# Performance work log

Hardware: AMD Instinct MI355X
Metric: run time of the kernel (lower is better)

Reference implementation:

```python
import jax, jax.numpy as jnp
import numpy as np

N_NODES = 200000
N_EDGES = 800000
N_GRAPHS = 4000
D_N = 35      # len(ATOM_VOCAB)=17 + 18
IN_CH = 8     # hardcoded in_channels
EMB = 256     # args.emb_size * 2
HID = 128     # args.emb_size (pred head hidden)


def setup_inputs() -> dict:
    key = jax.random.key(0)
    ks = jax.random.split(key, 16)
    s = lambda fan_in: 1.0 / np.sqrt(fan_in)
    x = jax.random.normal(ks[0], (N_NODES, D_N), dtype=jnp.float32)
    src = jax.random.randint(ks[1], (N_EDGES,), 0, N_NODES, dtype=jnp.int32)
    dst = jax.random.randint(ks[2], (N_EDGES,), 0, N_NODES, dtype=jnp.int32)
    seg = jnp.sort(jax.random.randint(ks[3], (N_NODES,), 0, N_GRAPHS, dtype=jnp.int32))
    return {
        "x": x, "src": src, "dst": dst, "seg": seg,
        # emb_linear (no bias): d_n -> 8
        "W_emb": jax.random.uniform(ks[4], (IN_CH, D_N), jnp.float32, -s(D_N), s(D_N)),
        # GCN layer 1: 8 -> 256 (agg='sum', residual=False)
        "W1": jax.random.uniform(ks[5], (EMB, IN_CH), jnp.float32, -s(IN_CH), s(IN_CH)),
        "b1": jnp.zeros((EMB,), jnp.float32),
        # GCN layers 2,3: 256 -> 256 (residual=True)
        "W2": jax.random.uniform(ks[6], (EMB, EMB), jnp.float32, -s(EMB), s(EMB)),
        "b2": jnp.zeros((EMB,), jnp.float32),
        "W3": jax.random.uniform(ks[7], (EMB, EMB), jnp.float32, -s(EMB), s(EMB)),
        "b3": jnp.zeros((EMB,), jnp.float32),
        # pred head: Linear(256,128,bias=False) -> ReLU -> Linear(128,1)
        "Wp1": jax.random.uniform(ks[8], (HID, EMB), jnp.float32, -s(EMB), s(EMB)),
        "Wp2": jax.random.uniform(ks[9], (1, HID), jnp.float32, -s(HID), s(HID)),
        "bp2": jnp.zeros((1,), jnp.float32),
    }


def _gcn_layer(h, src, dst, W, b, residual):
    # gather source node feats along edges, scatter-sum into destinations
    m = jax.ops.segment_sum(h[src], dst, num_segments=N_NODES)  # [N, d]
    out = jax.nn.relu(m @ W.T + b)
    return out + h if residual else out


def reference(x, src, dst, seg, W_emb, W1, b1, W2, b2, W3, b3, Wp1, Wp2, bp2):
    h = x @ W_emb.T                                   # [N, 8]
    h = _gcn_layer(h, src, dst, W1, b1, residual=False)  # [N, 256]
    h = _gcn_layer(h, src, dst, W2, b2, residual=True)
    h = _gcn_layer(h, src, dst, W3, b3, residual=True)
    g = jax.ops.segment_sum(h, seg, num_segments=N_GRAPHS)  # sum pooling [B, 256]
    pred = jax.nn.relu(g @ Wp1.T) @ Wp2.T + bp2       # [B, 1]
    return pred
```

## Files before the change

### kernel.cpp

```cpp
#include <hip/hip_runtime.h>
#include <hip/hip_bf16.h>

#define N_NODES 200000
#define N_EDGES 800000
#define N_GRAPHS 4000
#define D_N 35
#define IN_CH 8
#define EMB 256
#define HID 128

typedef unsigned short u16;
typedef __attribute__((ext_vector_type(8))) short bf16x8;
typedef __attribute__((ext_vector_type(8))) unsigned short ushort8;
typedef __attribute__((ext_vector_type(4))) float f32x4;

__device__ __forceinline__ float b2f(u16 u) {
    union { float f; unsigned v; } x; x.v = ((unsigned)u) << 16; return x.f;
}
__device__ __forceinline__ u16 f2b(float f) {
    union { float f; unsigned v; } x; x.f = f;
    unsigned r = x.v + 0x7fff + ((x.v >> 16) & 1);
    return (u16)(r >> 16);
}
#define RFL(v) __builtin_amdgcn_readfirstlane(v)


__global__ void count_deg(const int* __restrict__ dst, int* __restrict__ deg, int n) {
    int e = blockIdx.x * 256 + threadIdx.x;
    if (e < n) atomicAdd(&deg[dst[e]], 1);
}

__global__ __launch_bounds__(256) void scan_a(const int* __restrict__ deg, int* __restrict__ incl1,
                                              int* __restrict__ partials, int n) {
    __shared__ int s[256];
    int tid = threadIdx.x;
    int base = blockIdx.x * 1024;
    int v[4]; int sum = 0;
#pragma unroll
    for (int j = 0; j < 4; j++) {
        int idx = base + tid * 4 + j;
        v[j] = (idx < n) ? deg[idx] : 0;
        sum += v[j];
    }
    s[tid] = sum; __syncthreads();
    for (int off = 1; off < 256; off <<= 1) {
        int t = (tid >= off) ? s[tid - off] : 0;
        __syncthreads();
        s[tid] += t;
        __syncthreads();
    }
    int run = s[tid] - sum;
#pragma unroll
    for (int j = 0; j < 4; j++) {
        int idx = base + tid * 4 + j;
        run += v[j];
        if (idx < n) incl1[idx] = run;
    }
    if (tid == 255) partials[blockIdx.x] = s[255];
}

__global__ __launch_bounds__(256) void scan_b(int* __restrict__ partials, int np) {
    __shared__ int s[256];
    int tid = threadIdx.x;
    int v = (tid < np) ? partials[tid] : 0;
    s[tid] = v; __syncthreads();
    for (int off = 1; off < 256; off <<= 1) {
        int t = (tid >= off) ? s[tid - off] : 0;
        __syncthreads();
        s[tid] += t;
        __syncthreads();
    }
    if (tid < np) partials[tid] = s[tid] - v;
}

__global__ void scan_c(int* __restrict__ rowptr, const int* __restrict__ partials, int n) {
    int i = blockIdx.x * 256 + threadIdx.x;
    if (i < n) rowptr[1 + i] += partials[i >> 10];
    if (i == 0) rowptr[0] = 0;
}

__global__ void fill_csr(const int* __restrict__ src, const int* __restrict__ dst,
                         const int* __restrict__ rowptr, int* __restrict__ cursor,
                         int* __restrict__ csr, int n) {
    int e = blockIdx.x * 256 + threadIdx.x;
    if (e >= n) return;
    int d = dst[e];
    int p = atomicAdd(&cursor[d], 1);
    csr[rowptr[d] + p] = src[e];
}


__global__ __launch_bounds__(256) void swizzle_w(const float* __restrict__ W, u16* __restrict__ Wsw) {
    int t = blockIdx.x * 256 + threadIdx.x;
    int lane = t & 63;
    int n = ((t >> 9) << 4) + (lane & 15);
    int k0 = (((t >> 6) & 7) << 5) + ((lane >> 4) << 3);
    u16 v[8];
#pragma unroll
    for (int j = 0; j < 8; j++) v[j] = f2b(W[(size_t)n * 256 + k0 + j]);
    ushort4* o = (ushort4*)&Wsw[(size_t)t * 8];
    o[0] = make_ushort4(v[0], v[1], v[2], v[3]);
    o[1] = make_ushort4(v[4], v[5], v[6], v[7]);
}

__global__ __launch_bounds__(256) void swizzle_w1(const float* __restrict__ W1, u16* __restrict__ Wsw) {
    int t = blockIdx.x * 256 + threadIdx.x;
    int lane = t & 63;
    int nt = t >> 6;
    int n = nt * 16 + (lane & 15);
    int g = lane >> 4;
    u16 v[8];
#pragma unroll
    for (int j = 0; j < 8; j++) v[j] = (g == 0) ? f2b(W1[n * 8 + j]) : (u16)0;
    ushort4* o = (ushort4*)&Wsw[(size_t)t * 8];
    o[0] = make_ushort4(v[0], v[1], v[2], v[3]);
    o[1] = make_ushort4(v[4], v[5], v[6], v[7]);
}

__global__ __launch_bounds__(256) void emb8(const float* __restrict__ x, const float* __restrict__ We,
                                            u16* __restrict__ h0, int n) {
    __shared__ float ws[IN_CH * D_N];
    int tid = threadIdx.x;
    for (int i = tid; i < IN_CH * D_N; i += 256) ws[i] = We[i];
    __syncthreads();
    int node = blockIdx.x * 256 + tid;
    if (node >= n) return;
    float xr[D_N];
    const float* xp = &x[(size_t)node * D_N];
#pragma unroll
    for (int k = 0; k < D_N; k++) xr[k] = xp[k];
    ushort8 o;
#pragma unroll
    for (int j = 0; j < IN_CH; j++) {
        float acc = 0.f;
#pragma unroll
        for (int k = 0; k < D_N; k++) acc += xr[k] * ws[j * D_N + k];
        o[j] = f2b(acc);
    }
    *(ushort8*)&h0[(size_t)node * IN_CH] = o;
}

__global__ __launch_bounds__(256) void fused_l1(const u16* __restrict__ h0,
                                                const int* __restrict__ rowptr,
                                                const int* __restrict__ csr,
                                                const u16* __restrict__ Wsw1,
                                                const float* __restrict__ bias,
                                                u16* __restrict__ Hout) {
    __shared__ __attribute__((aligned(16))) u16 lds[16][256];
    const int wid = threadIdx.x >> 6;
    const int lane = threadIdx.x & 63;
    const int row0 = blockIdx.x * 16;
    char* ldsb = (char*)lds;
    const char* h0c = (const char*)h0;

    const int slot = lane >> 2;
    const int cid2 = (lane & 3) * 4;
    const int rbase = row0 + wid * 4;
    int s0 = RFL(rowptr[rbase + 0]);
    int s1 = RFL(rowptr[rbase + 1]);
    int s2 = RFL(rowptr[rbase + 2]);
    int s3 = RFL(rowptr[rbase + 3]);
    int s4 = RFL(rowptr[rbase + 4]);
    int es[5] = {s0, s1, s2, s3, s4};
#pragma unroll
    for (int r = 0; r < 4; r++) {
        int er = es[r], tr = es[r + 1];
        float2 acc = make_float2(0.f, 0.f);
        for (int eb = er; eb < tr; eb += 16) {
            int e = eb + slot;
            int ce = e < tr ? e : tr - 1;
            int sidx = csr[ce];
            unsigned v = *(const unsigned*)(h0c + (size_t)sidx * 16 + cid2);
            if (e < tr) {
                union { unsigned u; float f; } lo, hi;
                lo.u = v << 16; hi.u = v & 0xffff0000u;
                acc.x += lo.f; acc.y += hi.f;
            }
        }
        acc.x += __shfl_xor(acc.x, 4, 64);  acc.y += __shfl_xor(acc.y, 4, 64);
        acc.x += __shfl_xor(acc.x, 8, 64);  acc.y += __shfl_xor(acc.y, 8, 64);
        acc.x += __shfl_xor(acc.x, 16, 64); acc.y += __shfl_xor(acc.y, 16, 64);
        acc.x += __shfl_xor(acc.x, 32, 64); acc.y += __shfl_xor(acc.y, 32, 64);
        if (lane < 4) {
            unsigned pk = (unsigned)f2b(acc.x) | ((unsigned)f2b(acc.y) << 16);
            *(unsigned*)(ldsb + (wid * 4 + r) * 16 + cid2) = pk;
        }
    }
    __syncthreads();

    const int m = lane & 15;
    const int g = lane >> 4;
    bf16x8 a = {};
    if (g == 0) a = *(const bf16x8*)(ldsb + m * 16);
    __syncthreads();

    f32x4 acc[4];
#pragma unroll
    for (int t = 0; t < 4; t++) acc[t] = (f32x4){0.f, 0.f, 0.f, 0.f};
    const bf16x8* wp = (const bf16x8*)Wsw1 + lane;
#pragma unroll
    for (int t = 0; t < 4; t++) {
        bf16x8 b = wp[(wid * 4 + t) * 64];
        acc[t] = __builtin_amdgcn_mfma_f32_16x16x32_bf16(a, b, acc[t], 0, 0, 0);
    }

#pragma unroll
    for (int t = 0; t < 4; t++) {
        int col = (wid * 4 + t) * 16 + m;
#pragma unroll
        for (int r = 0; r < 4; r++) {
            int row = g * 4 + r;
            *(u16*)(ldsb + row * 512 + ((col * 2) ^ ((row & 7) << 4))) = f2b(acc[t][r]);
        }
    }
    __syncthreads();

    {
        int row = threadIdx.x >> 4;
        int cb0 = (threadIdx.x & 15) * 16;
#pragma unroll
        for (int p = 0; p < 2; p++) {
            int cb = cb0 + p * 256;
            ushort8 c = *(const ushort8*)(ldsb + row * 512 + (cb ^ ((row & 7) << 4)));
            int gcol = cb >> 1;
            size_t gidx = (size_t)(row0 + row) * EMB + gcol;
            float4 bq0 = *(const float4*)&bias[gcol];
            float4 bq1 = *(const float4*)&bias[gcol + 4];
            float bb[8] = {bq0.x, bq0.y, bq0.z, bq0.w, bq1.x, bq1.y, bq1.z, bq1.w};
            ushort8 o;
#pragma unroll
            for (int j = 0; j < 8; j++)
                o[j] = f2b(fmaxf(b2f(c[j]) + bb[j], 0.f));
            *(ushort8*)&Hout[gidx] = o;
        }
    }
}

__global__ __launch_bounds__(256, 8) void fused_gcn(const u16* __restrict__ Hin,
                                                    const int* __restrict__ rowptr,
                                                    const int* __restrict__ csr,
                                                    const u16* __restrict__ Wsw,
                                                    const float* __restrict__ bias,
                                                    u16* __restrict__ Hout) {
    __shared__ __attribute__((aligned(16))) u16 lds[16][256];
    const int wid = threadIdx.x >> 6;
    const int lane = threadIdx.x & 63;
    const int row0 = blockIdx.x * 16;
    char* ldsb = (char*)lds;
    const char* hbase = (const char*)Hin;
    const int laneByte = lane * 8;

    const int rbase = row0 + wid * 4;
    int e0 = RFL(rowptr[rbase + 0]);
    int t0 = RFL(rowptr[rbase + 1]);
    int t1 = RFL(rowptr[rbase + 2]);
    int t2 = RFL(rowptr[rbase + 3]);
    int t3 = RFL(rowptr[rbase + 4]);
    int e1 = t0, e2 = t1, e3 = t2;

    float2 acc[4][2];
#pragma unroll
    for (int r = 0; r < 4; r++) {
        acc[r][0] = make_float2(0.f, 0.f);
        acc[r][1] = make_float2(0.f, 0.f);
    }

    int ee[4] = {e0, e1, e2, e3};
    int tt[4] = {t0, t1, t2, t3};
    int idx[4][4];
#pragma unroll
    for (int r = 0; r < 4; r++) {
#pragma unroll
        for (int d = 0; d < 4; d++) {
            int ce = ee[r] + d;
            if (ce >= tt[r]) ce = tt[r] - 1;
            if (ce < 0) ce = 0;
            idx[r][d] = RFL(csr[ce]);
        }
    }

    while ((ee[0] < tt[0]) | (ee[1] < tt[1]) | (ee[2] < tt[2]) | (ee[3] < tt[3])) {
        uint2 val[4][4];
#pragma unroll
        for (int r = 0; r < 4; r++)
#pragma unroll
            for (int d = 0; d < 4; d++)
                val[r][d] = *(const uint2*)(hbase + (size_t)idx[r][d] * (EMB * 2) + laneByte);
        bool pr[4][4];
#pragma unroll
        for (int r = 0; r < 4; r++) {
#pragma unroll
            for (int d = 0; d < 4; d++) pr[r][d] = (ee[r] + d) < tt[r];
            ee[r] += 4;
#pragma unroll
            for (int d = 0; d < 4; d++) {
                int ce = ee[r] + d;
                if (ce >= tt[r]) ce = tt[r] - 1;
                if (ce < 0) ce = 0;
                idx[r][d] = RFL(csr[ce]);
            }
        }
#pragma unroll
        for (int r = 0; r < 4; r++)
#pragma unroll
            for (int d = 0; d < 4; d++)
                if (pr[r][d]) {
                    union { unsigned u; float f; } lo0, hi0, lo1, hi1;
                    lo0.u = val[r][d].x << 16; hi0.u = val[r][d].x & 0xffff0000u;
                    lo1.u = val[r][d].y << 16; hi1.u = val[r][d].y & 0xffff0000u;
                    acc[r][0].x += lo0.f; acc[r][0].y += hi0.f;
                    acc[r][1].x += lo1.f; acc[r][1].y += hi1.f;
                }
    }

#pragma unroll
    for (int r = 0; r < 4; r++) {
        int li = wid * 4 + r;
        unsigned px = (unsigned)f2b(acc[r][0].x) | ((unsigned)f2b(acc[r][0].y) << 16);
        unsigned py = (unsigned)f2b(acc[r][1].x) | ((unsigned)f2b(acc[r][1].y) << 16);
        *(uint2*)(ldsb + li * 512 + (laneByte ^ ((li & 7) << 4))) = make_uint2(px, py);
    }
    __syncthreads();

    const int m = lane & 15;
    const int g = lane >> 4;
    bf16x8 a[8];
#pragma unroll
    for (int ks = 0; ks < 8; ks++) {
        int boff = (g * 16 + ks * 64) ^ ((m & 7) << 4);
        a[ks] = *(const bf16x8*)(ldsb + m * 512 + boff);
    }
    __syncthreads();

    f32x4 acc2[4];
#pragma unroll
    for (int t = 0; t < 4; t++) acc2[t] = (f32x4){0.f, 0.f, 0.f, 0.f};
    const bf16x8* wp = (const bf16x8*)Wsw + lane;
#pragma unroll
    for (int t = 0; t < 4; t++) {
        int nt = wid * 4 + t;
        bf16x8 b[8];
#pragma unroll
        for (int ks = 0; ks < 8; ks++) b[ks] = wp[(nt * 8 + ks) * 64];
#pragma unroll
        for (int ks = 0; ks < 8; ks++)
            acc2[t] = __builtin_amdgcn_mfma_f32_16x16x32_bf16(a[ks], b[ks], acc2[t], 0, 0, 0);
    }

#pragma unroll
    for (int t = 0; t < 4; t++) {
        int col = (wid * 4 + t) * 16 + m;
#pragma unroll
        for (int r = 0; r < 4; r++) {
            int row = g * 4 + r;
            *(u16*)(ldsb + row * 512 + ((col * 2) ^ ((row & 7) << 4))) = f2b(acc2[t][r]);
        }
    }
    __syncthreads();

    {
        int row = threadIdx.x >> 4;
        int cb0 = (threadIdx.x & 15) * 16;
#pragma unroll
        for (int p = 0; p < 2; p++) {
            int cb = cb0 + p * 256;
            ushort8 c = *(const ushort8*)(ldsb + row * 512 + (cb ^ ((row & 7) << 4)));
            int gcol = cb >> 1;
            size_t gidx = (size_t)(row0 + row) * EMB + gcol;
            ushort8 hres = *(const ushort8*)&Hin[gidx];
            float4 bq0 = *(const float4*)&bias[gcol];
            float4 bq1 = *(const float4*)&bias[gcol + 4];
            float bb[8] = {bq0.x, bq0.y, bq0.z, bq0.w, bq1.x, bq1.y, bq1.z, bq1.w};
            ushort8 o;
#pragma unroll
            for (int j = 0; j < 8; j++)
                o[j] = f2b(fmaxf(b2f(c[j]) + bb[j], 0.f) + b2f(hres[j]));
            *(ushort8*)&Hout[gidx] = o;
        }
    }
}


__global__ void graph_bounds(const int* __restrict__ seg, int* __restrict__ gs, int n, int B) {
    int i = blockIdx.x * 256 + threadIdx.x;
    if (i >= n) return;
    int c = seg[i];
    int p = (i == 0) ? -1 : seg[i - 1];
    for (int b = p + 1; b <= c; b++) gs[b] = i;
    if (i == n - 1) {
        for (int b = c + 1; b <= B; b++) gs[b] = n;
    }
}

__global__ __launch_bounds__(256) void pool_head(const u16* __restrict__ h, const int* __restrict__ gs,
                                                 const float* __restrict__ Wp1, const float* __restrict__ Wp2,
                                                 const float* __restrict__ bp2, float* __restrict__ out) {
    __shared__ float gpq[4][EMB];
    __shared__ float gp[EMB];
    __shared__ float red[HID];
    int b = blockIdx.x, t = threadIdx.x;
    int s = gs[b], e = gs[b + 1];
    int q = t >> 6, ch4 = (t & 63) * 4;
    float a0 = 0.f, a1 = 0.f, a2 = 0.f, a3 = 0.f;
    int r = s + q;
    for (; r + 4 < e; r += 8) {
        ushort4 va = *(const ushort4*)&h[(size_t)r * EMB + ch4];
        ushort4 vb = *(const ushort4*)&h[(size_t)(r + 4) * EMB + ch4];
        a0 += b2f(va.x) + b2f(vb.x);
        a1 += b2f(va.y) + b2f(vb.y);
        a2 += b2f(va.z) + b2f(vb.z);
        a3 += b2f(va.w) + b2f(vb.w);
    }
    if (r < e) {
        ushort4 va = *(const ushort4*)&h[(size_t)r * EMB + ch4];
        a0 += b2f(va.x); a1 += b2f(va.y); a2 += b2f(va.z); a3 += b2f(va.w);
    }
    *(float4*)&gpq[q][ch4] = make_float4(a0, a1, a2, a3);
    __syncthreads();
    gp[t] = gpq[0][t] + gpq[1][t] + gpq[2][t] + gpq[3][t];
    __syncthreads();
    if (t < HID) {
        float acc = 0.f;
        const float4* wr = (const float4*)&Wp1[(size_t)t * EMB];
        const float4* gp4 = (const float4*)gp;
#pragma unroll 8
        for (int k = 0; k < EMB / 4; k++) {
            float4 w = wr[k], gg = gp4[k];
            acc += w.x * gg.x + w.y * gg.y + w.z * gg.z + w.w * gg.w;
        }
        red[t] = fmaxf(acc, 0.f) * Wp2[t];
    }
    __syncthreads();
    for (int off = 64; off > 0; off >>= 1) {
        if (t < off) red[t] += red[t + off];
        __syncthreads();
    }
    if (t == 0) out[b] = red[0] + bp2[0];
}


extern "C" void kernel_launch(void* const* d_in, const int* in_sizes, int n_in,
                              void* d_out, int out_size, void* d_ws, size_t ws_size,
                              hipStream_t stream) {
    const float* x    = (const float*)d_in[0];
    const int*   src  = (const int*)d_in[1];
    const int*   dst  = (const int*)d_in[2];
    const int*   seg  = (const int*)d_in[3];
    const float* W_emb= (const float*)d_in[4];
    const float* W1   = (const float*)d_in[5];
    const float* b1   = (const float*)d_in[6];
    const float* W2   = (const float*)d_in[7];
    const float* b2   = (const float*)d_in[8];
    const float* W3   = (const float*)d_in[9];
    const float* b3   = (const float*)d_in[10];
    const float* Wp1  = (const float*)d_in[11];
    const float* Wp2  = (const float*)d_in[12];
    const float* bp2  = (const float*)d_in[13];
    float* out = (float*)d_out;

    char* ws = (char*)d_ws;
    size_t off = 0;
    auto alloc = [&](size_t bytes) -> void* {
        void* p = ws + off;
        off = (off + bytes + 255) & ~(size_t)255;
        return p;
    };
    const int N = N_NODES, E = N_EDGES, G = N_GRAPHS;
    u16* hA     = (u16*)alloc((size_t)N * EMB * 2);
    u16* hB     = (u16*)alloc((size_t)N * EMB * 2);
    u16* h0     = (u16*)alloc((size_t)N * IN_CH * 2);
    u16* Wsw1   = (u16*)alloc(16 * 64 * 8 * 2);
    u16* Wsw2   = (u16*)alloc(256 * 256 * 2);
    u16* Wsw3   = (u16*)alloc(256 * 256 * 2);
    int* rowptr = (int*)alloc((size_t)(N + 1) * 4);
    int* deg    = (int*)alloc((size_t)N * 4);
    int* csr    = (int*)alloc((size_t)E * 4);
    int* partials = (int*)alloc(1024 * 4);
    int* gs     = (int*)alloc((size_t)(G + 1) * 4);

    if (off > ws_size) return;

    hipMemsetAsync(deg, 0, (size_t)N * 4, stream);
    count_deg<<<E / 256, 256, 0, stream>>>(dst, deg, E);
    scan_a<<<196, 256, 0, stream>>>(deg, rowptr + 1, partials, N);
    scan_b<<<1, 256, 0, stream>>>(partials, 196);
    scan_c<<<782, 256, 0, stream>>>(rowptr, partials, N);
    hipMemsetAsync(deg, 0, (size_t)N * 4, stream);
    fill_csr<<<E / 256, 256, 0, stream>>>(src, dst, rowptr, deg, csr, E);

    swizzle_w1<<<4, 256, 0, stream>>>(W1, Wsw1);
    swizzle_w<<<32, 256, 0, stream>>>(W2, Wsw2);
    swizzle_w<<<32, 256, 0, stream>>>(W3, Wsw3);

    emb8<<<782, 256, 0, stream>>>(x, W_emb, h0, N);
    fused_l1<<<N / 16, 256, 0, stream>>>(h0, rowptr, csr, Wsw1, b1, hA);

    fused_gcn<<<N / 16, 256, 0, stream>>>(hA, rowptr, csr, Wsw2, b2, hB);
    fused_gcn<<<N / 16, 256, 0, stream>>>(hB, rowptr, csr, Wsw3, b3, hA);

    graph_bounds<<<782, 256, 0, stream>>>(seg, gs, N, G);
    pool_head<<<G, 256, 0, stream>>>(hA, gs, Wp1, Wp2, bp2, out);
}
```

Baseline: 459.5 us.

## Flatten per-wave edge loop across four rows and drop redundant CSR memset

The gather loop in fused_gcn now walks the contiguous edge range of a wave's four rows as one stream, eight edges at a time, and routes each edge to the right row accumulator by comparing against row boundaries. The old loop advanced all four rows in lockstep, wasting slots when degrees differ. fill_csr now counts degrees down with atomicSub instead of using a re-zeroed cursor, which removes one memset. The two W2/W3 swizzle launches are merged into one. The per-edge branch chain adds some ALU work, and the CSR order within a row is reversed, which only changes the float summation order.

```diff
diff --git a/kernel.cpp b/kernel.cpp
--- a/kernel.cpp
+++ b/kernel.cpp
@@ -80,25 +80,29 @@
 }
 
 __global__ void fill_csr(const int* __restrict__ src, const int* __restrict__ dst,
-                         const int* __restrict__ rowptr, int* __restrict__ cursor,
+                         const int* __restrict__ rowptr, int* __restrict__ cnt,
                          int* __restrict__ csr, int n) {
     int e = blockIdx.x * 256 + threadIdx.x;
     if (e >= n) return;
     int d = dst[e];
-    int p = atomicAdd(&cursor[d], 1);
+    int p = atomicSub(&cnt[d], 1) - 1;
     csr[rowptr[d] + p] = src[e];
 }
 
 
-__global__ __launch_bounds__(256) void swizzle_w(const float* __restrict__ W, u16* __restrict__ Wsw) {
+__global__ __launch_bounds__(256) void swizzle_w23(const float* __restrict__ W2, const float* __restrict__ W3,
+                                                   u16* __restrict__ Wsw2, u16* __restrict__ Wsw3) {
     int t = blockIdx.x * 256 + threadIdx.x;
-    int lane = t & 63;
-    int n = ((t >> 9) << 4) + (lane & 15);
-    int k0 = (((t >> 6) & 7) << 5) + ((lane >> 4) << 3);
+    const float* W = (t < 8192) ? W2 : W3;
+    u16* Wsw = (t < 8192) ? Wsw2 : Wsw3;
+    int tl = t & 8191;
+    int lane = tl & 63;
+    int n = ((tl >> 9) << 4) + (lane & 15);
+    int k0 = (((tl >> 6) & 7) << 5) + ((lane >> 4) << 3);
     u16 v[8];
 #pragma unroll
     for (int j = 0; j < 8; j++) v[j] = f2b(W[(size_t)n * 256 + k0 + j]);
-    ushort4* o = (ushort4*)&Wsw[(size_t)t * 8];
+    ushort4* o = (ushort4*)&Wsw[(size_t)tl * 8];
     o[0] = make_ushort4(v[0], v[1], v[2], v[3]);
     o[1] = make_ushort4(v[4], v[5], v[6], v[7]);
 }
@@ -251,74 +255,62 @@
     const int laneByte = lane * 8;
 
     const int rbase = row0 + wid * 4;
-    int e0 = RFL(rowptr[rbase + 0]);
+    int s0 = RFL(rowptr[rbase + 0]);
     int t0 = RFL(rowptr[rbase + 1]);
     int t1 = RFL(rowptr[rbase + 2]);
     int t2 = RFL(rowptr[rbase + 3]);
     int t3 = RFL(rowptr[rbase + 4]);
-    int e1 = t0, e2 = t1, e3 = t2;
-
-    float2 acc[4][2];
-#pragma unroll
-    for (int r = 0; r < 4; r++) {
-        acc[r][0] = make_float2(0.f, 0.f);
-        acc[r][1] = make_float2(0.f, 0.f);
-    }
-
-    int ee[4] = {e0, e1, e2, e3};
-    int tt[4] = {t0, t1, t2, t3};
-    int idx[4][4];
-#pragma unroll
-    for (int r = 0; r < 4; r++) {
-#pragma unroll
-        for (int d = 0; d < 4; d++) {
-            int ce = ee[r] + d;
-            if (ce >= tt[r]) ce = tt[r] - 1;
+
+    float4 ar0 = make_float4(0.f, 0.f, 0.f, 0.f);
+    float4 ar1 = ar0, ar2 = ar0, ar3 = ar0;
+
+    int idx[8];
+#pragma unroll
+    for (int d = 0; d < 8; d++) {
+        int ce = s0 + d;
+        if (ce > t3 - 1) ce = t3 - 1;
+        if (ce < 0) ce = 0;
+        idx[d] = RFL(csr[ce]);
+    }
+    int ee = s0;
+    while (ee < t3) {
+        uint2 v[8];
+#pragma unroll
+        for (int d = 0; d < 8; d++)
+            v[d] = *(const uint2*)(hbase + (size_t)idx[d] * (EMB * 2) + laneByte);
+        int eb = ee;
+        ee += 8;
+#pragma unroll
+        for (int d = 0; d < 8; d++) {
+            int ce = ee + d;
+            if (ce > t3 - 1) ce = t3 - 1;
             if (ce < 0) ce = 0;
-            idx[r][d] = RFL(csr[ce]);
-        }
-    }
-
-    while ((ee[0] < tt[0]) | (ee[1] < tt[1]) | (ee[2] < tt[2]) | (ee[3] < tt[3])) {
-        uint2 val[4][4];
-#pragma unroll
-        for (int r = 0; r < 4; r++)
-#pragma unroll
-            for (int d = 0; d < 4; d++)
-                val[r][d] = *(const uint2*)(hbase + (size_t)idx[r][d] * (EMB * 2) + laneByte);
-        bool pr[4][4];
+            idx[d] = RFL(csr[ce]);
+        }
+#pragma unroll
+        for (int d = 0; d < 8; d++) {
+            int ed = eb + d;
+            if (ed < t3) {
+                union { unsigned u; float f; } l0, h0, l1, h1;
+                l0.u = v[d].x << 16; h0.u = v[d].x & 0xffff0000u;
+                l1.u = v[d].y << 16; h1.u = v[d].y & 0xffff0000u;
+                if (ed < t0)      { ar0.x += l0.f; ar0.y += h0.f; ar0.z += l1.f; ar0.w += h1.f; }
+                else if (ed < t1) { ar1.x += l0.f; ar1.y += h0.f; ar1.z += l1.f; ar1.w += h1.f; }
+                else if (ed < t2) { ar2.x += l0.f; ar2.y += h0.f; ar2.z += l1.f; ar2.w += h1.f; }
+                else              { ar3.x += l0.f; ar3.y += h0.f; ar3.z += l1.f; ar3.w += h1.f; }
+            }
+        }
+    }
+
+    {
+        float4 ars[4] = {ar0, ar1, ar2, ar3};
 #pragma unroll
         for (int r = 0; r < 4; r++) {
-#pragma unroll
-            for (int d = 0; d < 4; d++) pr[r][d] = (ee[r] + d) < tt[r];
-            ee[r] += 4;
-#pragma unroll
-            for (int d = 0; d < 4; d++) {
-                int ce = ee[r] + d;
-                if (ce >= tt[r]) ce = tt[r] - 1;
-                if (ce < 0) ce = 0;
-                idx[r][d] = RFL(csr[ce]);
-            }
-        }
-#pragma unroll
-        for (int r = 0; r < 4; r++)
-#pragma unroll
-            for (int d = 0; d < 4; d++)
-                if (pr[r][d]) {
-                    union { unsigned u; float f; } lo0, hi0, lo1, hi1;
-                    lo0.u = val[r][d].x << 16; hi0.u = val[r][d].x & 0xffff0000u;
-                    lo1.u = val[r][d].y << 16; hi1.u = val[r][d].y & 0xffff0000u;
-                    acc[r][0].x += lo0.f; acc[r][0].y += hi0.f;
-                    acc[r][1].x += lo1.f; acc[r][1].y += hi1.f;
-                }
-    }
-
-#pragma unroll
-    for (int r = 0; r < 4; r++) {
-        int li = wid * 4 + r;
-        unsigned px = (unsigned)f2b(acc[r][0].x) | ((unsigned)f2b(acc[r][0].y) << 16);
-        unsigned py = (unsigned)f2b(acc[r][1].x) | ((unsigned)f2b(acc[r][1].y) << 16);
-        *(uint2*)(ldsb + li * 512 + (laneByte ^ ((li & 7) << 4))) = make_uint2(px, py);
+            int li = wid * 4 + r;
+            unsigned px = (unsigned)f2b(ars[r].x) | ((unsigned)f2b(ars[r].y) << 16);
+            unsigned py = (unsigned)f2b(ars[r].z) | ((unsigned)f2b(ars[r].w) << 16);
+            *(uint2*)(ldsb + li * 512 + (laneByte ^ ((li & 7) << 4))) = make_uint2(px, py);
+        }
     }
     __syncthreads();
 
@@ -485,12 +477,10 @@
     scan_a<<<196, 256, 0, stream>>>(deg, rowptr + 1, partials, N);
     scan_b<<<1, 256, 0, stream>>>(partials, 196);
     scan_c<<<782, 256, 0, stream>>>(rowptr, partials, N);
-    hipMemsetAsync(deg, 0, (size_t)N * 4, stream);
     fill_csr<<<E / 256, 256, 0, stream>>>(src, dst, rowptr, deg, csr, E);
 
     swizzle_w1<<<4, 256, 0, stream>>>(W1, Wsw1);
-    swizzle_w<<<32, 256, 0, stream>>>(W2, Wsw2);
-    swizzle_w<<<32, 256, 0, stream>>>(W3, Wsw3);
+    swizzle_w23<<<64, 256, 0, stream>>>(W2, W3, Wsw2, Wsw3);
 
     emb8<<<782, 256, 0, stream>>>(x, W_emb, h0, N);
     fused_l1<<<N / 16, 256, 0, stream>>>(h0, rowptr, csr, Wsw1, b1, hA);
```

Result: faster. 446.0 us (-2.9%).
